# Kernel tuning notes

Hardware: AMD Instinct MI355X
Metric: run time of the kernel (lower is better)

Reference implementation:

```python
import jax, jax.numpy as jnp
import numpy as np

# db4 analysis filters (pywt.Wavelet('db4').dec_lo / dec_hi)
_DEC_LO = np.array([-0.010597401784997278, 0.032883011666982945, 0.030841381835986965,
                    -0.18703481171888114, -0.02798376941698385, 0.6308807679295904,
                    0.7148465705525415, 0.23037781330885523], dtype=np.float32)
_DEC_HI = np.array([-0.23037781330885523, 0.7148465705525415, -0.6308807679295904,
                    -0.02798376941698385, 0.18703481171888114, 0.030841381835986965,
                    -0.032883011666982945, -0.010597401784997278], dtype=np.float32)
# pytorch_wavelets stores filters reversed (torch conv = correlation); lax.conv is
# also correlation, so use the same reversed filters. Shape [2, 1, L].
_H = jnp.asarray(np.stack([_DEC_LO[::-1], _DEC_HI[::-1]])[:, None, :])

B, SW, SWS, HW, K, J = 2048, 4, 64, 8, 128, 3
DWT_LEN = 84  # 14 (lo, level 3) + 35 (hi1) + 21 (hi2) + 14 (hi3)


def _dwt_level(x, h):
    """One analysis level, mode='reflect' (pytorch_wavelets afb1d). x: [M, N]."""
    N = x.shape[-1]
    L = h.shape[-1]
    outsize = (N + L - 1) // 2          # pywt.dwt_coeff_len, non-periodization
    p = 2 * (outsize - 1) - N + L
    if p % 2 == 1:                       # odd total pad: one extra zero at the end
        x = jnp.pad(x, ((0, 0), (0, 1)))
    x = jnp.pad(x, ((0, 0), (p // 2, p // 2)), mode='reflect')
    y = jax.lax.conv_general_dilated(x[:, None, :], h, (2,), 'VALID')  # [M, 2, out]
    return y[:, 0, :], y[:, 1, :]


def setup_inputs() -> dict:
    key = jax.random.key(0)
    k1, k2, k3 = jax.random.split(key, 3)
    x = jax.random.normal(k1, (B, 1, SW * SWS, HW, HW), dtype=jnp.float32)
    # one Conv3d(1 -> K, kernel=(DWT_LEN, 8, 8)) per subwindow, kaiming-ish init
    fan_in = DWT_LEN * HW * HW
    conv_weight = jax.random.normal(k2, (SW, K, DWT_LEN, HW, HW), dtype=jnp.float32) / np.sqrt(fan_in)
    conv_bias = jax.random.normal(k3, (SW, K), dtype=jnp.float32) * 0.01
    return {"x": x, "conv_weight": conv_weight, "conv_bias": conv_bias}


def reference(x, conv_weight, conv_bias):
    b = x.shape[0]
    # [B,1,T,8,8] -> [B,SW,8,8,SWS]: DWT runs along the time axis of each subwindow
    xt = x[:, 0].reshape(b, SW, SWS, HW, HW).transpose(0, 1, 3, 4, 2)
    xm = xt.reshape(-1, SWS)  # [B*SW*64, 64]
    lo, highs = xm, []
    for _ in range(J):
        lo, hi = _dwt_level(lo, _H)
        highs.append(hi)
    coeffs = jnp.concatenate([lo] + highs, axis=-1)  # [M, 84], order: lo, hi1, hi2, hi3
    c = coeffs.reshape(b, SW, HW, HW, DWT_LEN).transpose(0, 1, 4, 2, 3)  # [B,SW,84,8,8]
    # per-subwindow Conv3d that fully reduces (t,h,w) -> [B, SW, K]
    feat = jnp.einsum('bsthw,skthw->bsk', c, conv_weight) + conv_bias[None]
    # Dropout3d is identity in eval; LeakyReLU default slope 0.01 (typo in source
    # means leakyrelu_negative_slope is never applied)
    return jax.nn.leaky_relu(feat, 0.01).reshape(b, SW * K)
```

## Files before the change

kernel.cpp:

```cpp
#include <hip/hip_runtime.h>
#include <stdint.h>

typedef unsigned int  u32;
typedef unsigned short u16;
typedef __bf16 bf16x8 __attribute__((ext_vector_type(8)));
typedef float  f32x4  __attribute__((ext_vector_type(4)));
typedef u32    u32x4  __attribute__((ext_vector_type(4)));

__constant__ float GL[8] = { 0.23037781330885523f,  0.7148465705525415f,
                             0.6308807679295904f,  -0.02798376941698385f,
                            -0.18703481171888114f,  0.030841381835986965f,
                             0.032883011666982945f,-0.010597401784997278f };
__constant__ float GH[8] = {-0.010597401784997278f,-0.032883011666982945f,
                             0.030841381835986965f, 0.18703481171888114f,
                            -0.02798376941698385f, -0.6308807679295904f,
                             0.7148465705525415f,  -0.23037781330885523f };

__device__ inline u16 f32_bf16(float f) {
    u32 u = __float_as_uint(f);
    u += 0x7fffu + ((u >> 16) & 1u);
    return (u16)(u >> 16);
}
__device__ inline u32 pack2_bf16(float a, float b) {
    u32 ua = __float_as_uint(a); ua += 0x7fffu + ((ua >> 16) & 1u);
    u32 ub = __float_as_uint(b); ub += 0x7fffu + ((ub >> 16) & 1u);
    return (ua >> 16) | (ub & 0xffff0000u);
}

__global__ __launch_bounds__(256) void fold_w(const float* __restrict__ cw,
                                              u16* __restrict__ Wf) {
    __shared__ float WdL[84 * 64];
    const int tid = threadIdx.x;

    if (tid < 64) {
        const int j = tid;
        float lo1[35], lo2[21];
#pragma unroll
        for (int i = 0; i < 35; ++i) {
            float sl = 0.f, sh = 0.f;
#pragma unroll
            for (int t = 0; t < 8; ++t) {
                int s = 2 * i + t - 6;
                if (s < 0) s = -s;
                if (s >= 64) s = 126 - s;
                float xv = (s == j) ? 1.0f : 0.0f;
                sl += xv * GL[t]; sh += xv * GH[t];
            }
            lo1[i] = sl;
            WdL[(14 + i) * 64 + j] = sh;
        }
#pragma unroll
        for (int i = 0; i < 21; ++i) {
            float sl = 0.f, sh = 0.f;
#pragma unroll
            for (int t = 0; t < 8; ++t) {
                int s = 2 * i + t - 6;
                if (s < 0) s = -s;
                if (s >= 36) s = 70 - s;
                float xv = (s >= 35) ? 0.0f : lo1[s];
                sl += xv * GL[t]; sh += xv * GH[t];
            }
            lo2[i] = sl;
            WdL[(49 + i) * 64 + j] = sh;
        }
#pragma unroll
        for (int i = 0; i < 14; ++i) {
            float sl = 0.f, sh = 0.f;
#pragma unroll
            for (int t = 0; t < 8; ++t) {
                int s = 2 * i + t - 6;
                if (s < 0) s = -s;
                if (s >= 22) s = 42 - s;
                float xv = (s >= 21) ? 0.0f : lo2[s];
                sl += xv * GL[t]; sh += xv * GH[t];
            }
            WdL[i * 64 + j] = sl;
            WdL[(70 + i) * 64 + j] = sh;
        }
    }
    __syncthreads();

    const int sk = blockIdx.x;
    const int s  = sk >> 7;
    const int n  = sk & 127;
    const int hw = tid & 63;
    const int tg = __builtin_amdgcn_readfirstlane((int)(tid >> 6));
    const int t0 = tg * 16;
    const float* wk = cw + (size_t)sk * (84 * 64);
    float acc[16];
#pragma unroll
    for (int j = 0; j < 16; ++j) acc[j] = 0.f;
#pragma unroll 4
    for (int tau = 0; tau < 84; ++tau) {
        float wv = wk[tau * 64 + hw];
        const float* Wr = WdL + tau * 64 + t0;
#pragma unroll
        for (int j = 0; j < 16; ++j) acc[j] += wv * Wr[j];
    }
    const int nt = n >> 4;
    const int fr = n & 15;
    const int fq = (hw >> 3) & 3;
    const int jj = hw & 7;
    const int kbh = hw >> 5;
#pragma unroll
    for (int j = 0; j < 16; ++j) {
        const int t = t0 + j;
        const size_t idx =
            ((((size_t)(s * 8 + nt)) * 128 + t * 2 + kbh) * 64 + fq * 16 + fr) * 8 + jj;
        Wf[idx] = f32_bf16(acc[j]);
    }
}

template <int NKB>
__global__ __launch_bounds__(256, 3) void gemm2(const float* __restrict__ X,
                                                const u16* __restrict__ Wf,
                                                float* __restrict__ P) {
    const int tid  = threadIdx.x;
    const int lane = tid & 63;
    const int gw   = blockIdx.x * 4 + (tid >> 6);
    const int ksid = gw >> 9;
    const int rem  = gw & 511;
    const int s    = rem >> 7;
    const int mt   = rem & 127;
    const int fr   = lane & 15;
    const int fq   = lane >> 4;
    const int kb0  = ksid * NKB;

    const float* xg = X + (size_t)(mt * 16 + fr) * 16384 + s * 4096 + kb0 * 32 + fq * 8;
    const u16*   wg = Wf + (((size_t)(s * 8) * 128) + kb0) * 512 + lane * 8;

    f32x4 acc[8];
#pragma unroll
    for (int nt = 0; nt < 8; ++nt) acc[nt] = (f32x4){0.f, 0.f, 0.f, 0.f};

    f32x4 a0 = __builtin_nontemporal_load(reinterpret_cast<const f32x4*>(xg));
    f32x4 a1 = __builtin_nontemporal_load(reinterpret_cast<const f32x4*>(xg) + 1);

#pragma unroll 2
    for (int kb = 0; kb < NKB; ++kb) {
        union { u32 u[4]; bf16x8 v; } av;
        av.u[0] = pack2_bf16(a0.x, a0.y); av.u[1] = pack2_bf16(a0.z, a0.w);
        av.u[2] = pack2_bf16(a1.x, a1.y); av.u[3] = pack2_bf16(a1.z, a1.w);
        const int kn = (kb + 1 < NKB) ? kb + 1 : kb;
        a0 = __builtin_nontemporal_load(reinterpret_cast<const f32x4*>(xg + (size_t)kn * 32));
        a1 = __builtin_nontemporal_load(reinterpret_cast<const f32x4*>(xg + (size_t)kn * 32) + 1);
        const u16* wb = wg + (size_t)kb * 512;
#pragma unroll
        for (int nt = 0; nt < 8; ++nt) {
            bf16x8 bf = *reinterpret_cast<const bf16x8*>(wb + (size_t)nt * 65536);
            acc[nt] = __builtin_amdgcn_mfma_f32_16x16x32_bf16(av.v, bf, acc[nt], 0, 0, 0);
        }
    }

    float* pg = P + (size_t)ksid * (2048 * 512) + (size_t)(mt * 16) * 512 + s * 128 + fr;
#pragma unroll
    for (int nt = 0; nt < 8; ++nt)
#pragma unroll
        for (int r = 0; r < 4; ++r)
            __builtin_nontemporal_store(acc[nt][r], pg + (size_t)(fq * 4 + r) * 512 + nt * 16);
}

__global__ __launch_bounds__(256) void reduce_k(const float* __restrict__ P,
                                                const float* __restrict__ bias,
                                                float* __restrict__ out, int nks) {
    const int t = blockIdx.x * 256 + threadIdx.x;
    const size_t base = (size_t)t * 4;
    f32x4 sum = {0.f, 0.f, 0.f, 0.f};
    for (int k = 0; k < nks; ++k) {
        f32x4 v = __builtin_nontemporal_load(
            reinterpret_cast<const f32x4*>(P + (size_t)k * (2048 * 512) + base));
        sum += v;
    }
    const f32x4 b = *reinterpret_cast<const f32x4*>(bias + (base & 511));
    f32x4 o = sum + b;
    o.x = o.x > 0.f ? o.x : 0.01f * o.x;
    o.y = o.y > 0.f ? o.y : 0.01f * o.y;
    o.z = o.z > 0.f ? o.z : 0.01f * o.z;
    o.w = o.w > 0.f ? o.w : 0.01f * o.w;
    __builtin_nontemporal_store(o, reinterpret_cast<f32x4*>(out + base));
}

extern "C" void kernel_launch(void* const* d_in, const int* in_sizes, int n_in,
                              void* d_out, int out_size, void* d_ws, size_t ws_size,
                              hipStream_t stream) {
    const float* x  = (const float*)d_in[0];
    const float* cw = (const float*)d_in[1];
    const float* cb = (const float*)d_in[2];
    float* out = (float*)d_out;

    u16*   Wf = (u16*)d_ws;
    float* P  = (float*)((char*)d_ws + (4u << 20));

    const size_t MN = (size_t)2048 * 512 * 4;
    int ks = (ws_size >= (4u << 20) + 8 * MN) ? 8
           : (ws_size >= (4u << 20) + 4 * MN) ? 4
           : (ws_size >= (4u << 20) + 2 * MN) ? 2 : 1;

    fold_w<<<512, 256, 0, stream>>>(cw, Wf);
    switch (ks) {
        case 8: gemm2<16> <<<128 * 8, 256, 0, stream>>>(x, Wf, P); break;
        case 4: gemm2<32> <<<128 * 4, 256, 0, stream>>>(x, Wf, P); break;
        case 2: gemm2<64> <<<128 * 2, 256, 0, stream>>>(x, Wf, P); break;
        default: gemm2<128><<<128 * 1, 256, 0, stream>>>(x, Wf, P); break;
    }
    reduce_k<<<1024, 256, 0, stream>>>(P, cb, out, ks);
}
```

Baseline: 246.1 us.

## Double per-wave M tile in GEMM and compute DWT fold matrix per thread

The GEMM now has each wave process two 16-row M tiles that share every loaded weight fragment, which halves weight reads per MFMA and halves the grid size. The trade-off is double the accumulator registers, so launch bounds drop to 2 blocks per SM. fold_w no longer builds the DWT matrix in shared memory with one wave and a barrier. Every thread now computes its own 84-entry DWT column in registers, reads conv weights for 16 hw positions, and writes packed bf16 words instead of scalar u16 stores. This costs redundant DWT arithmetic across the four waves and more register pressure.

```diff
diff --git a/kernel.cpp b/kernel.cpp
--- a/kernel.cpp
+++ b/kernel.cpp
@@ -5,7 +5,6 @@
 typedef unsigned short u16;
 typedef __bf16 bf16x8 __attribute__((ext_vector_type(8)));
 typedef float  f32x4  __attribute__((ext_vector_type(4)));
-typedef u32    u32x4  __attribute__((ext_vector_type(4)));
 
 __constant__ float GL[8] = { 0.23037781330885523f,  0.7148465705525415f,
                              0.6308807679295904f,  -0.02798376941698385f,
@@ -29,135 +28,146 @@
 
 __global__ __launch_bounds__(256) void fold_w(const float* __restrict__ cw,
                                               u16* __restrict__ Wf) {
-    __shared__ float WdL[84 * 64];
     const int tid = threadIdx.x;
-
-    if (tid < 64) {
-        const int j = tid;
-        float lo1[35], lo2[21];
-#pragma unroll
-        for (int i = 0; i < 35; ++i) {
-            float sl = 0.f, sh = 0.f;
-#pragma unroll
-            for (int t = 0; t < 8; ++t) {
-                int s = 2 * i + t - 6;
-                if (s < 0) s = -s;
-                if (s >= 64) s = 126 - s;
-                float xv = (s == j) ? 1.0f : 0.0f;
-                sl += xv * GL[t]; sh += xv * GH[t];
-            }
-            lo1[i] = sl;
-            WdL[(14 + i) * 64 + j] = sh;
-        }
-#pragma unroll
-        for (int i = 0; i < 21; ++i) {
-            float sl = 0.f, sh = 0.f;
-#pragma unroll
-            for (int t = 0; t < 8; ++t) {
-                int s = 2 * i + t - 6;
-                if (s < 0) s = -s;
-                if (s >= 36) s = 70 - s;
-                float xv = (s >= 35) ? 0.0f : lo1[s];
-                sl += xv * GL[t]; sh += xv * GH[t];
-            }
-            lo2[i] = sl;
-            WdL[(49 + i) * 64 + j] = sh;
-        }
-#pragma unroll
-        for (int i = 0; i < 14; ++i) {
-            float sl = 0.f, sh = 0.f;
-#pragma unroll
-            for (int t = 0; t < 8; ++t) {
-                int s = 2 * i + t - 6;
-                if (s < 0) s = -s;
-                if (s >= 22) s = 42 - s;
-                float xv = (s >= 21) ? 0.0f : lo2[s];
-                sl += xv * GL[t]; sh += xv * GH[t];
-            }
-            WdL[i * 64 + j] = sl;
-            WdL[(70 + i) * 64 + j] = sh;
-        }
-    }
-    __syncthreads();
+    const int t   = tid & 63;
+    const int wq  = __builtin_amdgcn_readfirstlane((int)(tid >> 6));
+
+    float wd[84], lo1[35], lo2[21];
+#pragma unroll
+    for (int i = 0; i < 35; ++i) {
+        float sl = 0.f, sh = 0.f;
+#pragma unroll
+        for (int k = 0; k < 8; ++k) {
+            int s = 2 * i + k - 6;
+            if (s < 0) s = -s;
+            if (s >= 64) s = 126 - s;
+            float xv = (s == t) ? 1.0f : 0.0f;
+            sl += xv * GL[k]; sh += xv * GH[k];
+        }
+        lo1[i] = sl;
+        wd[14 + i] = sh;
+    }
+#pragma unroll
+    for (int i = 0; i < 21; ++i) {
+        float sl = 0.f, sh = 0.f;
+#pragma unroll
+        for (int k = 0; k < 8; ++k) {
+            int s = 2 * i + k - 6;
+            if (s < 0) s = -s;
+            if (s >= 36) s = 70 - s;
+            float xv = (s >= 35) ? 0.0f : lo1[s];
+            sl += xv * GL[k]; sh += xv * GH[k];
+        }
+        lo2[i] = sl;
+        wd[49 + i] = sh;
+    }
+#pragma unroll
+    for (int i = 0; i < 14; ++i) {
+        float sl = 0.f, sh = 0.f;
+#pragma unroll
+        for (int k = 0; k < 8; ++k) {
+            int s = 2 * i + k - 6;
+            if (s < 0) s = -s;
+            if (s >= 22) s = 42 - s;
+            float xv = (s >= 21) ? 0.0f : lo2[s];
+            sl += xv * GL[k]; sh += xv * GH[k];
+        }
+        wd[i] = sl;
+        wd[70 + i] = sh;
+    }
 
     const int sk = blockIdx.x;
+    const float* cwp = cw + (size_t)sk * (84 * 64) + wq * 16;
+    float acc[16];
+#pragma unroll
+    for (int j = 0; j < 16; ++j) acc[j] = 0.f;
+#pragma unroll
+    for (int tau = 0; tau < 84; ++tau) {
+#pragma unroll
+        for (int j = 0; j < 16; ++j)
+            acc[j] += cwp[tau * 64 + j] * wd[tau];
+    }
+
     const int s  = sk >> 7;
     const int n  = sk & 127;
-    const int hw = tid & 63;
-    const int tg = __builtin_amdgcn_readfirstlane((int)(tid >> 6));
-    const int t0 = tg * 16;
-    const float* wk = cw + (size_t)sk * (84 * 64);
-    float acc[16];
-#pragma unroll
-    for (int j = 0; j < 16; ++j) acc[j] = 0.f;
-#pragma unroll 4
-    for (int tau = 0; tau < 84; ++tau) {
-        float wv = wk[tau * 64 + hw];
-        const float* Wr = WdL + tau * 64 + t0;
-#pragma unroll
-        for (int j = 0; j < 16; ++j) acc[j] += wv * Wr[j];
-    }
     const int nt = n >> 4;
     const int fr = n & 15;
-    const int fq = (hw >> 3) & 3;
-    const int jj = hw & 7;
-    const int kbh = hw >> 5;
-#pragma unroll
-    for (int j = 0; j < 16; ++j) {
-        const int t = t0 + j;
+#pragma unroll
+    for (int h8 = 0; h8 < 2; ++h8) {
+        const int hw0 = wq * 16 + h8 * 8;
+        const int kb  = t * 2 + (hw0 >> 5);
+        const int fq  = (hw0 >> 3) & 3;
+        union { u16 h[8]; u32 w2[4]; } pk;
+#pragma unroll
+        for (int j = 0; j < 8; ++j) pk.h[j] = f32_bf16(acc[h8 * 8 + j]);
         const size_t idx =
-            ((((size_t)(s * 8 + nt)) * 128 + t * 2 + kbh) * 64 + fq * 16 + fr) * 8 + jj;
-        Wf[idx] = f32_bf16(acc[j]);
+            ((((size_t)(s * 8 + nt)) * 128 + kb) * 64 + fq * 16 + fr) * 8;
+        *reinterpret_cast<u32*>(&Wf[idx])     = pk.w2[0];
+        *reinterpret_cast<u32*>(&Wf[idx + 2]) = pk.w2[1];
+        *reinterpret_cast<u32*>(&Wf[idx + 4]) = pk.w2[2];
+        *reinterpret_cast<u32*>(&Wf[idx + 6]) = pk.w2[3];
     }
 }
 
 template <int NKB>
-__global__ __launch_bounds__(256, 3) void gemm2(const float* __restrict__ X,
+__global__ __launch_bounds__(256, 2) void gemm3(const float* __restrict__ X,
                                                 const u16* __restrict__ Wf,
                                                 float* __restrict__ P) {
     const int tid  = threadIdx.x;
     const int lane = tid & 63;
     const int gw   = blockIdx.x * 4 + (tid >> 6);
-    const int ksid = gw >> 9;
-    const int rem  = gw & 511;
-    const int s    = rem >> 7;
-    const int mt   = rem & 127;
+    const int ksid = gw >> 8;
+    const int s    = (gw >> 6) & 3;
+    const int mt   = gw & 63;
     const int fr   = lane & 15;
     const int fq   = lane >> 4;
     const int kb0  = ksid * NKB;
 
-    const float* xg = X + (size_t)(mt * 16 + fr) * 16384 + s * 4096 + kb0 * 32 + fq * 8;
-    const u16*   wg = Wf + (((size_t)(s * 8) * 128) + kb0) * 512 + lane * 8;
-
-    f32x4 acc[8];
-#pragma unroll
-    for (int nt = 0; nt < 8; ++nt) acc[nt] = (f32x4){0.f, 0.f, 0.f, 0.f};
-
-    f32x4 a0 = __builtin_nontemporal_load(reinterpret_cast<const f32x4*>(xg));
-    f32x4 a1 = __builtin_nontemporal_load(reinterpret_cast<const f32x4*>(xg) + 1);
+    const float* xg0 = X + (size_t)(mt * 32 + fr) * 16384 + s * 4096 + kb0 * 32 + fq * 8;
+    const float* xg1 = xg0 + (size_t)16 * 16384;
+    const u16*   wg  = Wf + (((size_t)(s * 8) * 128) + kb0) * 512 + lane * 8;
+
+    f32x4 acc0[8], acc1[8];
+#pragma unroll
+    for (int nt = 0; nt < 8; ++nt) {
+        acc0[nt] = (f32x4){0.f, 0.f, 0.f, 0.f};
+        acc1[nt] = (f32x4){0.f, 0.f, 0.f, 0.f};
+    }
+
+    f32x4 a0 = __builtin_nontemporal_load(reinterpret_cast<const f32x4*>(xg0));
+    f32x4 a1 = __builtin_nontemporal_load(reinterpret_cast<const f32x4*>(xg0) + 1);
+    f32x4 a2 = __builtin_nontemporal_load(reinterpret_cast<const f32x4*>(xg1));
+    f32x4 a3 = __builtin_nontemporal_load(reinterpret_cast<const f32x4*>(xg1) + 1);
 
 #pragma unroll 2
     for (int kb = 0; kb < NKB; ++kb) {
-        union { u32 u[4]; bf16x8 v; } av;
-        av.u[0] = pack2_bf16(a0.x, a0.y); av.u[1] = pack2_bf16(a0.z, a0.w);
-        av.u[2] = pack2_bf16(a1.x, a1.y); av.u[3] = pack2_bf16(a1.z, a1.w);
+        union { u32 u[4]; bf16x8 v; } av0, av1;
+        av0.u[0] = pack2_bf16(a0.x, a0.y); av0.u[1] = pack2_bf16(a0.z, a0.w);
+        av0.u[2] = pack2_bf16(a1.x, a1.y); av0.u[3] = pack2_bf16(a1.z, a1.w);
+        av1.u[0] = pack2_bf16(a2.x, a2.y); av1.u[1] = pack2_bf16(a2.z, a2.w);
+        av1.u[2] = pack2_bf16(a3.x, a3.y); av1.u[3] = pack2_bf16(a3.z, a3.w);
         const int kn = (kb + 1 < NKB) ? kb + 1 : kb;
-        a0 = __builtin_nontemporal_load(reinterpret_cast<const f32x4*>(xg + (size_t)kn * 32));
-        a1 = __builtin_nontemporal_load(reinterpret_cast<const f32x4*>(xg + (size_t)kn * 32) + 1);
+        a0 = __builtin_nontemporal_load(reinterpret_cast<const f32x4*>(xg0 + (size_t)kn * 32));
+        a1 = __builtin_nontemporal_load(reinterpret_cast<const f32x4*>(xg0 + (size_t)kn * 32) + 1);
+        a2 = __builtin_nontemporal_load(reinterpret_cast<const f32x4*>(xg1 + (size_t)kn * 32));
+        a3 = __builtin_nontemporal_load(reinterpret_cast<const f32x4*>(xg1 + (size_t)kn * 32) + 1);
         const u16* wb = wg + (size_t)kb * 512;
 #pragma unroll
         for (int nt = 0; nt < 8; ++nt) {
             bf16x8 bf = *reinterpret_cast<const bf16x8*>(wb + (size_t)nt * 65536);
-            acc[nt] = __builtin_amdgcn_mfma_f32_16x16x32_bf16(av.v, bf, acc[nt], 0, 0, 0);
-        }
-    }
-
-    float* pg = P + (size_t)ksid * (2048 * 512) + (size_t)(mt * 16) * 512 + s * 128 + fr;
+            acc0[nt] = __builtin_amdgcn_mfma_f32_16x16x32_bf16(av0.v, bf, acc0[nt], 0, 0, 0);
+            acc1[nt] = __builtin_amdgcn_mfma_f32_16x16x32_bf16(av1.v, bf, acc1[nt], 0, 0, 0);
+        }
+    }
+
+    float* pg = P + (size_t)ksid * (2048 * 512) + (size_t)(mt * 32) * 512 + s * 128 + fr;
 #pragma unroll
     for (int nt = 0; nt < 8; ++nt)
 #pragma unroll
-        for (int r = 0; r < 4; ++r)
-            __builtin_nontemporal_store(acc[nt][r], pg + (size_t)(fq * 4 + r) * 512 + nt * 16);
+        for (int r = 0; r < 4; ++r) {
+            __builtin_nontemporal_store(acc0[nt][r], pg + (size_t)(fq * 4 + r) * 512 + nt * 16);
+            __builtin_nontemporal_store(acc1[nt][r], pg + (size_t)(16 + fq * 4 + r) * 512 + nt * 16);
+        }
 }
 
 __global__ __launch_bounds__(256) void reduce_k(const float* __restrict__ P,
@@ -198,10 +208,10 @@
 
     fold_w<<<512, 256, 0, stream>>>(cw, Wf);
     switch (ks) {
-        case 8: gemm2<16> <<<128 * 8, 256, 0, stream>>>(x, Wf, P); break;
-        case 4: gemm2<32> <<<128 * 4, 256, 0, stream>>>(x, Wf, P); break;
-        case 2: gemm2<64> <<<128 * 2, 256, 0, stream>>>(x, Wf, P); break;
-        default: gemm2<128><<<128 * 1, 256, 0, stream>>>(x, Wf, P); break;
+        case 8: gemm3<16> <<<8 * 64, 256, 0, stream>>>(x, Wf, P); break;
+        case 4: gemm3<32> <<<4 * 64, 256, 0, stream>>>(x, Wf, P); break;
+        case 2: gemm3<64> <<<2 * 64, 256, 0, stream>>>(x, Wf, P); break;
+        default: gemm3<128><<<1 * 64, 256, 0, stream>>>(x, Wf, P); break;
     }
     reduce_k<<<1024, 256, 0, stream>>>(P, cb, out, ks);
 }
```

New measurement: 299.4 us. 21.7% more time.
